# Optimization experiments

Measured on AMD Instinct MI355X. Metric: run time of the kernel, lower is better.

## Reference

```python
import jax, jax.numpy as jnp
import numpy as np

HIDDEN = 2048
N_HEADS = 32
N_KV_HEADS = 8
HEAD_DIM = HIDDEN // N_HEADS  # 64
ROPE_BASE = 10000.0
B, S = 2, 2048
NEG_INF = -1e9


def rotate_half(x):
    x1, x2 = jnp.split(x, 2, axis=-1)
    return jnp.concatenate((-x2, x1), axis=-1)


def rope_cos_sin(seq_len, head_dim, base, dtype):
    inv_freq = 1.0 / (base ** (jnp.arange(0, head_dim, 2, dtype=jnp.float32) / head_dim))
    pos = jnp.arange(seq_len, dtype=jnp.float32)
    freqs = jnp.outer(pos, inv_freq)              # [S, D/2]
    emb = jnp.concatenate((freqs, freqs), axis=-1)  # [S, D]
    return jnp.cos(emb).astype(dtype)[None, None], jnp.sin(emb).astype(dtype)[None, None]


def setup_inputs() -> dict:
    key = jax.random.key(0)
    ks = jax.random.split(key, 5)
    hidden_states = jax.random.normal(ks[0], (B, S, HIDDEN), dtype=jnp.float32)
    # causal additive mask, Llama-style
    causal = jnp.tril(jnp.ones((S, S), dtype=bool))
    attention_mask = jnp.where(causal, 0.0, NEG_INF).astype(jnp.float32)
    attention_mask = jnp.broadcast_to(attention_mask[None, None], (B, 1, S, S))
    sc = 1.0 / np.sqrt(HIDDEN)
    Wq = jax.random.normal(ks[1], (HIDDEN, HIDDEN), dtype=jnp.float32) * sc
    Wk = jax.random.normal(ks[2], (N_KV_HEADS * HEAD_DIM, HIDDEN), dtype=jnp.float32) * sc
    Wv = jax.random.normal(ks[3], (N_KV_HEADS * HEAD_DIM, HIDDEN), dtype=jnp.float32) * sc
    Wo = jax.random.normal(ks[4], (HIDDEN, HIDDEN), dtype=jnp.float32) * sc
    return {"hidden_states": hidden_states, "attention_mask": attention_mask,
            "Wq": Wq, "Wk": Wk, "Wv": Wv, "Wo": Wo}


def reference(hidden_states, attention_mask, Wq, Wk, Wv, Wo):
    b, s, _ = hidden_states.shape
    groups = N_HEADS // N_KV_HEADS
    # projections (torch Linear: x @ W.T)
    q = (hidden_states @ Wq.T).reshape(b, s, N_HEADS, HEAD_DIM).transpose(0, 2, 1, 3)      # [b,H,s,d]
    k = (hidden_states @ Wk.T).reshape(b, s, N_KV_HEADS, HEAD_DIM).transpose(0, 2, 1, 3)   # [b,Hk,s,d]
    v = (hidden_states @ Wv.T).reshape(b, s, N_KV_HEADS, HEAD_DIM).transpose(0, 2, 1, 3)
    cos, sin = rope_cos_sin(s, HEAD_DIM, ROPE_BASE, hidden_states.dtype)
    q = q * cos + rotate_half(q) * sin
    k = k * cos + rotate_half(k) * sin
    # GQA without materializing repeated K/V: view q as [b, Hk, g, s, d]
    qg = q.reshape(b, N_KV_HEADS, groups, s, HEAD_DIM)
    scores = jnp.einsum('bhgqd,bhkd->bhgqk', qg, k) / np.sqrt(HEAD_DIM)  # [b,Hk,g,s,s]
    scores = scores + attention_mask[:, :, None]                          # mask [b,1,1,s,s]
    probs = jax.nn.softmax(scores.astype(jnp.float32), axis=-1).astype(q.dtype)
    attn = jnp.einsum('bhgqk,bhkd->bhgqd', probs, v)                      # [b,Hk,g,s,d]
    attn = attn.reshape(b, N_HEADS, s, HEAD_DIM).transpose(0, 2, 1, 3).reshape(b, s, HIDDEN)
    return attn @ Wo.T
```

## Files before the change

kernel.cpp:

```cpp
#include <hip/hip_runtime.h>
#include <math.h>

#define HID 2048
#define NH 32
#define NKV 8
#define HD 64
#define BB 2
#define SS 2048
#define MTOT (BB * SS)

typedef __bf16 bf16;
typedef __bf16 bf16x8 __attribute__((ext_vector_type(8)));
typedef __bf16 bf16x4 __attribute__((ext_vector_type(4)));
typedef float f32x4 __attribute__((ext_vector_type(4)));

#define MFMA16(a, b, c) __builtin_amdgcn_mfma_f32_16x16x32_bf16((a), (b), (c), 0, 0, 0)

__device__ __forceinline__ void load_lds16(const void* g, void* l) {
  __builtin_amdgcn_global_load_lds((const __attribute__((address_space(1))) void*)g,
                                   (__attribute__((address_space(3))) void*)l, 16, 0, 0);
}

#define FENCE() asm volatile("" ::: "memory")
#define SYNC_VM(N) do { FENCE(); \
  asm volatile("s_waitcnt vmcnt(" #N ") lgkmcnt(0)" ::: "memory"); \
  __builtin_amdgcn_s_barrier(); FENCE(); } while (0)

__global__ void cvt_all(const float* __restrict__ hs, const float* __restrict__ Wq,
                        const float* __restrict__ Wk, const float* __restrict__ Wv,
                        const float* __restrict__ Wo,
                        bf16* __restrict__ A_b, bf16* __restrict__ Wq_b,
                        bf16* __restrict__ Wk_b, bf16* __restrict__ Wv_b,
                        bf16* __restrict__ Wo_b) {
  int bid = blockIdx.x;
  const float* src;
  bf16* dst;
  if (bid < 8192)       { src = hs; dst = A_b; }
  else if (bid < 12288) { src = Wq; dst = Wq_b; bid -= 8192; }
  else if (bid < 13312) { src = Wk; dst = Wk_b; bid -= 12288; }
  else if (bid < 14336) { src = Wv; dst = Wv_b; bid -= 13312; }
  else                  { src = Wo; dst = Wo_b; bid -= 14336; }
  int i = (bid * 256 + threadIdx.x) * 4;
  float4 v = *(const float4*)(src + i);
  bf16x4 o;
  o[0] = (bf16)v.x; o[1] = (bf16)v.y; o[2] = (bf16)v.z; o[3] = (bf16)v.w;
  *(bf16x4*)(dst + i) = o;
}

__device__ __forceinline__ void gemm_core256x128(const char* Agc, const char* Bgc,
                                                 char* lds, f32x4 (&acc)[4][4]) {
  constexpr int ABYTES = 16384;
  constexpr int BUFB = 24576;
  constexpr int NT = HID / 32;

  const int tid = threadIdx.x;
  const int w = tid >> 6, lane = tid & 63;
  const int l16 = lane & 15, quad = lane >> 4;
  const int wr = w >> 1, wc = w & 1;
  const int wb = w * 1024;

  const int cu = (tid & 7) ^ ((tid >> 3) & 7);
  const int srcR0 = 2 * (tid >> 3) + (cu >> 2);
  const int srcC = (cu & 3) * 16;
  const char* gA = Agc + (size_t)srcR0 * (HID * 2) + srcC;
  const char* gB = Bgc + (size_t)srcR0 * (HID * 2) + srcC;

  const int acg16 = ((((l16 & 1) << 2) | quad) ^ ((l16 >> 1) & 7)) * 16;
  const int aoff = (wr * 32 + (l16 >> 1)) * 128 + acg16;
  const int boff = ABYTES + (wc * 32 + (l16 >> 1)) * 128 + acg16;

#pragma unroll
  for (int t0 = 0; t0 < 2; ++t0) {
    char* lb = lds + t0 * BUFB;
    load_lds16(gA + t0 * 64, lb + wb);
    load_lds16(gA + (size_t)128 * (HID * 2) + t0 * 64, lb + 8192 + wb);
    load_lds16(gB + t0 * 64, lb + ABYTES + wb);
  }

  char* cur = lds;
  char* stg = lds + 2 * BUFB;
  for (int kt = 0; kt < NT; ++kt) {
    SYNC_VM(3);
    const int ks = (kt + 2 < NT) ? (kt + 2) * 64 : (NT - 1) * 64;

    load_lds16(gA + ks, stg + wb);
    load_lds16(gA + (size_t)128 * (HID * 2) + ks, stg + 8192 + wb);
    load_lds16(gB + ks, stg + ABYTES + wb);
    FENCE();

    bf16x8 af[4], bfr[4];
#pragma unroll
    for (int ni = 0; ni < 4; ++ni)
      bfr[ni] = *(const bf16x8*)(cur + boff + ni * 1024);
#pragma unroll
    for (int mi = 0; mi < 4; ++mi)
      af[mi] = *(const bf16x8*)(cur + aoff + mi * 1024);
    __builtin_amdgcn_s_setprio(1);
#pragma unroll
    for (int mi = 0; mi < 4; ++mi)
#pragma unroll
      for (int ni = 0; ni < 4; ++ni)
        acc[mi][ni] = MFMA16(af[mi], bfr[ni], acc[mi][ni]);
    __builtin_amdgcn_s_setprio(0);

    cur = (cur == lds + 2 * BUFB) ? lds : cur + BUFB;
    stg = (stg == lds + 2 * BUFB) ? lds : stg + BUFB;
  }
  asm volatile("s_waitcnt vmcnt(0)" ::: "memory");
}

#define QSCALE 0.1803368801f
#define L2B 0.4152410118f
__global__ __launch_bounds__(512, 4) void gemm_qkv(const bf16* __restrict__ A,
                                                   const bf16* __restrict__ Wq,
                                                   const bf16* __restrict__ Wk,
                                                   const bf16* __restrict__ Wv,
                                                   bf16* __restrict__ Qb,
                                                   bf16* __restrict__ Kb,
                                                   bf16* __restrict__ Vt) {
  __shared__ __align__(16) char lds[3 * 24576];
  const int tileM = blockIdx.x * 256;
  const int n0 = blockIdx.y * 128;
  const bf16* Wp;
  int mode;
  if (n0 < HID) { Wp = Wq + (size_t)n0 * HID; mode = 0; }
  else if (n0 < HID + 512) { Wp = Wk + (size_t)(n0 - HID) * HID; mode = 1; }
  else { Wp = Wv + (size_t)(n0 - HID - 512) * HID; mode = 2; }

  f32x4 acc[4][4];
#pragma unroll
  for (int i = 0; i < 4; ++i)
#pragma unroll
    for (int j = 0; j < 4; ++j) acc[i][j] = (f32x4){0.f, 0.f, 0.f, 0.f};

  gemm_core256x128((const char*)(A + (size_t)tileM * HID), (const char*)Wp, lds, acc);

  const int tid = threadIdx.x;
  const int w = tid >> 6, lane = tid & 63;
  const int l16 = lane & 15, quad = lane >> 4;
  const int wr = w >> 1, wc = w & 1;
  const int mbase = tileM + wr * 64;
  const int cb = n0 + wc * 64;

  if (mode == 2) {
#pragma unroll
    for (int mi = 0; mi < 4; ++mi)
#pragma unroll
      for (int ni = 0; ni < 4; ++ni)
#pragma unroll
        for (int r = 0; r < 4; ++r) {
          int grow = mbase + mi * 16 + quad * 4 + r;
          int b = grow >> 11, spos = grow & (SS - 1);
          int nv = cb + ni * 16 + l16 - (HID + 512);
          Vt[(((size_t)(b * NKV + (nv >> 6))) * HD + (nv & 63)) * SS + spos] =
              (bf16)acc[mi][ni][r];
        }
  } else {
    const float inv0 = __builtin_amdgcn_exp2f(-(float)l16 * L2B);
    const float inv1 = __builtin_amdgcn_exp2f(-(float)(l16 + 16) * L2B);
#pragma unroll
    for (int mi = 0; mi < 4; ++mi) {
#pragma unroll
      for (int r = 0; r < 4; ++r) {
        int grow = mbase + mi * 16 + quad * 4 + r;
        int b = grow >> 11, spos = grow & (SS - 1);
        float sn0, cs0, sn1, cs1;
        sincosf((float)spos * inv0, &sn0, &cs0);
        sincosf((float)spos * inv1, &sn1, &cs1);
        float a0 = acc[mi][0][r], a1 = acc[mi][1][r];
        float a2 = acc[mi][2][r], a3 = acc[mi][3][r];
        float o0 = a0 * cs0 - a2 * sn0;
        float o2 = a2 * cs0 + a0 * sn0;
        float o1 = a1 * cs1 - a3 * sn1;
        float o3 = a3 * cs1 + a1 * sn1;
        if (mode == 0) {
          bf16* qp = Qb + (size_t)grow * HID + cb + l16;
          qp[0]  = (bf16)(o0 * QSCALE);
          qp[16] = (bf16)(o1 * QSCALE);
          qp[32] = (bf16)(o2 * QSCALE);
          qp[48] = (bf16)(o3 * QSCALE);
        } else {
          int kvh = (cb - HID) >> 6;
          bf16* kp = Kb + ((size_t)(b * NKV + kvh) * SS + spos) * HD + l16;
          kp[0]  = (bf16)o0;
          kp[16] = (bf16)o1;
          kp[32] = (bf16)o2;
          kp[48] = (bf16)o3;
        }
      }
    }
  }
}

__global__ __launch_bounds__(512, 4) void gemm_out(const bf16* __restrict__ A,
                                                   const bf16* __restrict__ Wo,
                                                   float* __restrict__ out) {
  __shared__ __align__(16) char lds[3 * 24576];
  const int tileM = blockIdx.x * 256;
  const int n0 = blockIdx.y * 128;
  f32x4 acc[4][4];
#pragma unroll
  for (int i = 0; i < 4; ++i)
#pragma unroll
    for (int j = 0; j < 4; ++j) acc[i][j] = (f32x4){0.f, 0.f, 0.f, 0.f};

  gemm_core256x128((const char*)(A + (size_t)tileM * HID),
                   (const char*)(Wo + (size_t)n0 * HID), lds, acc);

  const int tid = threadIdx.x;
  const int w = tid >> 6, lane = tid & 63;
  const int l16 = lane & 15, quad = lane >> 4;
  const int wr = w >> 1, wc = w & 1;
#pragma unroll
  for (int mi = 0; mi < 4; ++mi)
#pragma unroll
    for (int ni = 0; ni < 4; ++ni)
#pragma unroll
      for (int r = 0; r < 4; ++r) {
        int grow = tileM + wr * 64 + mi * 16 + quad * 4 + r;
        int gcol = n0 + wc * 64 + ni * 16 + l16;
        out[(size_t)grow * HID + gcol] = acc[mi][ni][r];
      }
}

#define PSTR 72
__global__ __launch_bounds__(256, 3) void attn(const bf16* __restrict__ Qb,
                                               const bf16* __restrict__ Kb,
                                               const bf16* __restrict__ Vt,
                                               bf16* __restrict__ Ctx) {
  __shared__ bf16 Ktile[2][64 * 64];
  __shared__ bf16 Vtile[2][64 * 64];
  __shared__ bf16 Pbuf[4][32 * PSTR];
  const int tid = threadIdx.x;
  const int w = tid >> 6, lane = tid & 63;
  const int l16 = lane & 15, quad = lane >> 4;
  const int bh = blockIdx.y, b = bh >> 5, h = bh & 31, kvh = h >> 2;
  bf16* Pw = &Pbuf[w][0];
  const char* Kslice = (const char*)(Kb + ((size_t)(b * NKV + kvh)) * SS * HD);
  const char* Vslice = (const char*)(Vt + ((size_t)(b * NKV + kvh)) * HD * SS);
  const int qrel = w * 16 + l16;

  const int srow = (lane >> 3) & 7;
  const int pchunk = ((lane & 7) ^ srow) << 4;
  const int so = ((quad ^ (l16 & 7)) << 4);
  const int so2 = so ^ 64;

  const int xA = (int)blockIdx.x;

  int cur = 0;
  {
#pragma unroll
    for (int i = 0; i < 2; ++i) {
      const int r = w * 16 + i * 8 + srow;
      load_lds16(Kslice + (size_t)r * 128 + pchunk,
                 (char*)Ktile[0] + (w * 16 + i * 8) * 128);
      load_lds16(Vslice + (size_t)r * 4096 + pchunk,
                 (char*)Vtile[0] + (w * 16 + i * 8) * 128);
    }
  }

  for (int t = 0; t < 2; ++t) {
    const int X = t ? (15 - xA) : xA;
    const int qA = X * 128 + qrel;
    const int ktmax = 2 * X + 1;

    const bf16* QpA = Qb + ((size_t)(b * SS + qA)) * HID + h * HD + quad * 8;
    bf16x8 qa0 = *(const bf16x8*)QpA;
    bf16x8 qa1 = *(const bf16x8*)(QpA + 32);
    const bf16* QpB = QpA + (size_t)64 * HID;
    bf16x8 qbB0 = *(const bf16x8*)QpB;
    bf16x8 qbB1 = *(const bf16x8*)(QpB + 32);

    float lA = 0.f, lB = 0.f;
    f32x4 oA[4], oB[4];
#pragma unroll
    for (int d = 0; d < 4; ++d) {
      oA[d] = (f32x4){0.f, 0.f, 0.f, 0.f};
      oB[d] = (f32x4){0.f, 0.f, 0.f, 0.f};
    }

    for (int kt = 0; kt <= ktmax; ++kt) {
      __syncthreads();

      const bool have_next = (kt < ktmax) || (t == 0);
      if (have_next) {
        const int nkb = (kt < ktmax) ? (kt + 1) * 64 : 0;
        const int nb = cur ^ 1;
#pragma unroll
        for (int i = 0; i < 2; ++i) {
          const int r = w * 16 + i * 8 + srow;
          load_lds16(Kslice + (size_t)(nkb + r) * 128 + pchunk,
                     (char*)Ktile[nb] + (w * 16 + i * 8) * 128);
          load_lds16(Vslice + (size_t)r * 4096 + (size_t)nkb * 2 + pchunk,
                     (char*)Vtile[nb] + (w * 16 + i * 8) * 128);
        }
      }

      const char* Kc = (const char*)Ktile[cur] + l16 * 128;
      const char* Vc = (const char*)Vtile[cur] + l16 * 128;
      const bool skipA = (kt == ktmax);
      const bool diagA = (kt == ktmax - 1);
      const bool diagB = (kt == ktmax);

#pragma unroll
      for (int nt = 0; nt < 4; ++nt) {
        bf16x8 kf0 = *(const bf16x8*)(Kc + nt * 2048 + so);
        bf16x8 kf1 = *(const bf16x8*)(Kc + nt * 2048 + so2);
        const int krel = nt * 16 + quad * 4;

        bf16x4 pkA;
        if (skipA) {
          pkA[0] = (bf16)0.f; pkA[1] = (bf16)0.f;
          pkA[2] = (bf16)0.f; pkA[3] = (bf16)0.f;
        } else {
          f32x4 s = {0.f, 0.f, 0.f, 0.f};
          s = MFMA16(kf0, qa0, s);
          s = MFMA16(kf1, qa1, s);
          if (diagA) {
#pragma unroll
            for (int r = 0; r < 4; ++r) {
              float p = (krel + r > qrel) ? 0.f : __builtin_amdgcn_exp2f(s[r]);
              lA += p;
              pkA[r] = (bf16)p;
            }
          } else {
#pragma unroll
            for (int r = 0; r < 4; ++r) {
              float p = __builtin_amdgcn_exp2f(s[r]);
              lA += p;
              pkA[r] = (bf16)p;
            }
          }
        }
        *(bf16x4*)&Pw[l16 * PSTR + krel] = pkA;

        f32x4 sB = {0.f, 0.f, 0.f, 0.f};
        sB = MFMA16(kf0, qbB0, sB);
        sB = MFMA16(kf1, qbB1, sB);
        bf16x4 pkB;
        if (diagB) {
#pragma unroll
          for (int r = 0; r < 4; ++r) {
            float p = (krel + r > qrel) ? 0.f : __builtin_amdgcn_exp2f(sB[r]);
            lB += p;
            pkB[r] = (bf16)p;
          }
        } else {
#pragma unroll
          for (int r = 0; r < 4; ++r) {
            float p = __builtin_amdgcn_exp2f(sB[r]);
            lB += p;
            pkB[r] = (bf16)p;
          }
        }
        *(bf16x4*)&Pw[(16 + l16) * PSTR + krel] = pkB;
      }

      bf16x8 pA0 = *(const bf16x8*)&Pw[l16 * PSTR + quad * 8];
      bf16x8 pA1 = *(const bf16x8*)&Pw[l16 * PSTR + 32 + quad * 8];
      bf16x8 pB0 = *(const bf16x8*)&Pw[(16 + l16) * PSTR + quad * 8];
      bf16x8 pB1 = *(const bf16x8*)&Pw[(16 + l16) * PSTR + 32 + quad * 8];
#pragma unroll
      for (int dn = 0; dn < 4; ++dn) {
        bf16x8 v0 = *(const bf16x8*)(Vc + dn * 2048 + so);
        bf16x8 v1 = *(const bf16x8*)(Vc + dn * 2048 + so2);
        oA[dn] = MFMA16(v0, pA0, oA[dn]);
        oA[dn] = MFMA16(v1, pA1, oA[dn]);
        oB[dn] = MFMA16(v0, pB0, oB[dn]);
        oB[dn] = MFMA16(v1, pB1, oB[dn]);
      }
      cur ^= 1;
    }

    lA += __shfl_xor(lA, 16);
    lA += __shfl_xor(lA, 32);
    lB += __shfl_xor(lB, 16);
    lB += __shfl_xor(lB, 32);
    const float invA = 1.0f / lA;
    const float invB = 1.0f / lB;
    bf16* CpA = Ctx + ((size_t)(b * SS + qA)) * HID + h * HD + quad * 4;
    bf16* CpB = CpA + (size_t)64 * HID;
#pragma unroll
    for (int dn = 0; dn < 4; ++dn) {
      bf16x4 ovA, ovB;
#pragma unroll
      for (int r = 0; r < 4; ++r) {
        ovA[r] = (bf16)(oA[dn][r] * invA);
        ovB[r] = (bf16)(oB[dn][r] * invB);
      }
      *(bf16x4*)(CpA + dn * 16) = ovA;
      *(bf16x4*)(CpB + dn * 16) = ovB;
    }
  }
}

extern "C" void kernel_launch(void* const* d_in, const int* in_sizes, int n_in,
                              void* d_out, int out_size, void* d_ws, size_t ws_size,
                              hipStream_t stream) {
  const float* hs = (const float*)d_in[0];
  const float* Wq = (const float*)d_in[2];
  const float* Wk = (const float*)d_in[3];
  const float* Wv = (const float*)d_in[4];
  const float* Wo = (const float*)d_in[5];

  char* ws = (char*)d_ws;
  bf16* A_b  = (bf16*)(ws);
  bf16* Wq_b = (bf16*)(ws + 16777216);
  bf16* Wk_b = (bf16*)(ws + 25165824);
  bf16* Wv_b = (bf16*)(ws + 27262976);
  bf16* Wo_b = (bf16*)(ws + 29360128);
  bf16* Qb   = (bf16*)(ws + 37748736);
  bf16* Kb   = (bf16*)(ws + 54525952);
  bf16* Vt   = (bf16*)(ws + 58720256);
  bf16* Ctx  = A_b;

  cvt_all<<<18432, 256, 0, stream>>>(hs, Wq, Wk, Wv, Wo, A_b, Wq_b, Wk_b, Wv_b, Wo_b);
  gemm_qkv<<<dim3(MTOT / 256, 24), 512, 0, stream>>>(A_b, Wq_b, Wk_b, Wv_b, Qb, Kb, Vt);
  attn<<<dim3(8, BB * NH), 256, 0, stream>>>(Qb, Kb, Vt, Ctx);
  gemm_out<<<dim3(MTOT / 256, HID / 128), 512, 0, stream>>>(Ctx, Wo_b, (float*)d_out);
}
```

Before: 298.5 us.

## Double GEMM K-step to 64 with new LDS layout and swizzle

Rewrites the shared GEMM core so each pipeline stage loads a K=64 slice instead of K=32. This halves the number of barrier/wait iterations and issues two MFMAs per accumulator per stage. It uses a new row-major, XOR-swizzled LDS layout with six async global-to-LDS loads per stage. LDS per block doubles to 144 KB, so launch bounds drop to 2 blocks per CU, which lowers occupancy and latency hiding.

```diff
diff --git a/kernel.cpp b/kernel.cpp
--- a/kernel.cpp
+++ b/kernel.cpp
@@ -47,11 +47,11 @@
   *(bf16x4*)(dst + i) = o;
 }
 
-__device__ __forceinline__ void gemm_core256x128(const char* Agc, const char* Bgc,
-                                                 char* lds, f32x4 (&acc)[4][4]) {
-  constexpr int ABYTES = 16384;
-  constexpr int BUFB = 24576;
-  constexpr int NT = HID / 32;
+__device__ __forceinline__ void gemm_core_k64(const char* Agc, const char* Bgc,
+                                              char* lds, f32x4 (&acc)[4][4]) {
+  constexpr int ABYTES = 32768;
+  constexpr int BUFB = 49152;
+  constexpr int NT = HID / 64;
 
   const int tid = threadIdx.x;
   const int w = tid >> 6, lane = tid & 63;
@@ -59,48 +59,63 @@
   const int wr = w >> 1, wc = w & 1;
   const int wb = w * 1024;
 
-  const int cu = (tid & 7) ^ ((tid >> 3) & 7);
-  const int srcR0 = 2 * (tid >> 3) + (cu >> 2);
-  const int srcC = (cu & 3) * 16;
-  const char* gA = Agc + (size_t)srcR0 * (HID * 2) + srcC;
-  const char* gB = Bgc + (size_t)srcR0 * (HID * 2) + srcC;
-
-  const int acg16 = ((((l16 & 1) << 2) | quad) ^ ((l16 >> 1) & 7)) * 16;
-  const int aoff = (wr * 32 + (l16 >> 1)) * 128 + acg16;
-  const int boff = ABYTES + (wc * 32 + (l16 >> 1)) * 128 + acg16;
+  const int cu = (lane & 7) ^ ((lane >> 3) & 7);
+  const char* gA = Agc + (size_t)(w * 8 + (lane >> 3)) * 4096 + cu * 16;
+  const char* gB = Bgc + (size_t)(w * 8 + (lane >> 3)) * 4096 + cu * 16;
+
+  const int aswz = l16 & 7;
+  const int a_k0 = ((0 + quad) ^ aswz) * 16;
+  const int a_k1 = ((4 + quad) ^ aswz) * 16;
+  const int arow = (wr * 64 + l16) * 128;
+  const int brow = (wc * 64 + l16) * 128;
 
 #pragma unroll
   for (int t0 = 0; t0 < 2; ++t0) {
     char* lb = lds + t0 * BUFB;
-    load_lds16(gA + t0 * 64, lb + wb);
-    load_lds16(gA + (size_t)128 * (HID * 2) + t0 * 64, lb + 8192 + wb);
-    load_lds16(gB + t0 * 64, lb + ABYTES + wb);
+#pragma unroll
+    for (int j = 0; j < 4; ++j)
+      load_lds16(gA + (size_t)j * (64 * 4096) + t0 * 128, lb + wb + j * 8192);
+#pragma unroll
+    for (int j = 0; j < 2; ++j)
+      load_lds16(gB + (size_t)j * (64 * 4096) + t0 * 128, lb + ABYTES + wb + j * 8192);
   }
 
   char* cur = lds;
   char* stg = lds + 2 * BUFB;
   for (int kt = 0; kt < NT; ++kt) {
-    SYNC_VM(3);
-    const int ks = (kt + 2 < NT) ? (kt + 2) * 64 : (NT - 1) * 64;
-
-    load_lds16(gA + ks, stg + wb);
-    load_lds16(gA + (size_t)128 * (HID * 2) + ks, stg + 8192 + wb);
-    load_lds16(gB + ks, stg + ABYTES + wb);
+    SYNC_VM(6);
+    const int ks = (kt + 2 < NT) ? (kt + 2) : (NT - 1);
+    const size_t ko = (size_t)ks * 128;
+
+#pragma unroll
+    for (int j = 0; j < 4; ++j)
+      load_lds16(gA + (size_t)j * (64 * 4096) + ko, stg + wb + j * 8192);
+#pragma unroll
+    for (int j = 0; j < 2; ++j)
+      load_lds16(gB + (size_t)j * (64 * 4096) + ko, stg + ABYTES + wb + j * 8192);
     FENCE();
 
-    bf16x8 af[4], bfr[4];
-#pragma unroll
-    for (int ni = 0; ni < 4; ++ni)
-      bfr[ni] = *(const bf16x8*)(cur + boff + ni * 1024);
+    const char* Ac = cur;
+    const char* Bc = cur + ABYTES;
+    bf16x8 af0[4], af1[4], bf0[4], bf1[4];
+#pragma unroll
+    for (int ni = 0; ni < 4; ++ni) {
+      bf0[ni] = *(const bf16x8*)(Bc + brow + ni * 2048 + a_k0);
+      bf1[ni] = *(const bf16x8*)(Bc + brow + ni * 2048 + a_k1);
+    }
+#pragma unroll
+    for (int mi = 0; mi < 4; ++mi) {
+      af0[mi] = *(const bf16x8*)(Ac + arow + mi * 2048 + a_k0);
+      af1[mi] = *(const bf16x8*)(Ac + arow + mi * 2048 + a_k1);
+    }
+    __builtin_amdgcn_s_setprio(1);
 #pragma unroll
     for (int mi = 0; mi < 4; ++mi)
-      af[mi] = *(const bf16x8*)(cur + aoff + mi * 1024);
-    __builtin_amdgcn_s_setprio(1);
-#pragma unroll
-    for (int mi = 0; mi < 4; ++mi)
-#pragma unroll
-      for (int ni = 0; ni < 4; ++ni)
-        acc[mi][ni] = MFMA16(af[mi], bfr[ni], acc[mi][ni]);
+#pragma unroll
+      for (int ni = 0; ni < 4; ++ni) {
+        acc[mi][ni] = MFMA16(af0[mi], bf0[ni], acc[mi][ni]);
+        acc[mi][ni] = MFMA16(af1[mi], bf1[ni], acc[mi][ni]);
+      }
     __builtin_amdgcn_s_setprio(0);
 
     cur = (cur == lds + 2 * BUFB) ? lds : cur + BUFB;
@@ -111,14 +126,14 @@
 
 #define QSCALE 0.1803368801f
 #define L2B 0.4152410118f
-__global__ __launch_bounds__(512, 4) void gemm_qkv(const bf16* __restrict__ A,
+__global__ __launch_bounds__(512, 2) void gemm_qkv(const bf16* __restrict__ A,
                                                    const bf16* __restrict__ Wq,
                                                    const bf16* __restrict__ Wk,
                                                    const bf16* __restrict__ Wv,
                                                    bf16* __restrict__ Qb,
                                                    bf16* __restrict__ Kb,
                                                    bf16* __restrict__ Vt) {
-  __shared__ __align__(16) char lds[3 * 24576];
+  __shared__ __align__(16) char lds[3 * 49152];
   const int tileM = blockIdx.x * 256;
   const int n0 = blockIdx.y * 128;
   const bf16* Wp;
@@ -133,7 +148,7 @@
 #pragma unroll
     for (int j = 0; j < 4; ++j) acc[i][j] = (f32x4){0.f, 0.f, 0.f, 0.f};
 
-  gemm_core256x128((const char*)(A + (size_t)tileM * HID), (const char*)Wp, lds, acc);
+  gemm_core_k64((const char*)(A + (size_t)tileM * HID), (const char*)Wp, lds, acc);
 
   const int tid = threadIdx.x;
   const int w = tid >> 6, lane = tid & 63;
@@ -192,10 +207,10 @@
   }
 }
 
-__global__ __launch_bounds__(512, 4) void gemm_out(const bf16* __restrict__ A,
+__global__ __launch_bounds__(512, 2) void gemm_out(const bf16* __restrict__ A,
                                                    const bf16* __restrict__ Wo,
                                                    float* __restrict__ out) {
-  __shared__ __align__(16) char lds[3 * 24576];
+  __shared__ __align__(16) char lds[3 * 49152];
   const int tileM = blockIdx.x * 256;
   const int n0 = blockIdx.y * 128;
   f32x4 acc[4][4];
@@ -204,8 +219,8 @@
 #pragma unroll
     for (int j = 0; j < 4; ++j) acc[i][j] = (f32x4){0.f, 0.f, 0.f, 0.f};
 
-  gemm_core256x128((const char*)(A + (size_t)tileM * HID),
-                   (const char*)(Wo + (size_t)n0 * HID), lds, acc);
+  gemm_core_k64((const char*)(A + (size_t)tileM * HID),
+                (const char*)(Wo + (size_t)n0 * HID), lds, acc);
 
   const int tid = threadIdx.x;
   const int w = tid >> 6, lane = tid & 63;
```

Result: no change. 296.7 us (-0.6%).
